# Kernel optimization log

Hardware: AMD Instinct MI355X
Metric: run time of the kernel (lower is better)

The kernel has to match this reference:

```python
import jax, jax.numpy as jnp
import numpy as np

CELL = 4  # 2 ** cell_2_pow, cell_2_pow = 2
EPS = 1e-5


def conv2d(x, w, b):
    # 3x3 conv, padding 1, NCHW / OIHW
    y = jax.lax.conv_general_dilated(
        x, w, window_strides=(1, 1), padding=((1, 1), (1, 1)),
        dimension_numbers=('NCHW', 'OIHW', 'NCHW'))
    return y + b[None, :, None, None]


def setup_inputs() -> dict:
    key = jax.random.key(0)
    ks = jax.random.split(key, 4)
    B, Cc, H, W = 8, 128, 512, 512
    nh, nw = H // CELL, W // CELL  # ctrl spatial must be padded_img / cell_sz
    return dict(
        image_pipe=jax.random.normal(ks[0], (B, 6, H, W), jnp.float32),
        ctrl_pipe=jax.random.normal(ks[1], (B, Cc, nh, nw), jnp.float32),
        w1=jax.random.normal(ks[2], (50, Cc, 3, 3), jnp.float32) * 0.03,
        b1=jnp.zeros((50,), jnp.float32),
        gamma=jnp.ones((50,), jnp.float32),
        beta=jnp.zeros((50,), jnp.float32),
        mean=jnp.zeros((50,), jnp.float32),
        var=jnp.ones((50,), jnp.float32),
        w2=jax.random.normal(ks[3], (18, 50, 3, 3), jnp.float32) * 0.05,
        b2=jnp.zeros((18,), jnp.float32),
    )


def reference(image_pipe, ctrl_pipe, w1, b1, gamma, beta, mean, var, w2, b2):
    cs = CELL
    B, C6, H, W = image_pipe.shape
    # conv_condense: Conv(Cc->50) -> ReLU -> BatchNorm2d(50, inference) -> Conv(50->18)
    h = jax.nn.relu(conv2d(ctrl_pipe, w1, b1))
    scale = gamma * jax.lax.rsqrt(var + EPS)
    h = (h - mean[None, :, None, None]) * scale[None, :, None, None] + beta[None, :, None, None]
    cond = conv2d(h, w2, b2)  # [B, 18, nh, nw]
    nh, nw = cond.shape[-2], cond.shape[-1]

    padH = (-H) % cs
    padW = (-W) % cs
    rH, rW = H + padH, W + padW
    # F.pad(img, (cell, padW+cell, cell, padH+cell)): left/right then top/bottom
    img = jnp.pad(image_pipe, ((0, 0), (0, 0), (cs, padH + cs), (cs, padW + cs)))

    # 9 cell-strided shifted views; torch loop order: i over width (outer), j over height (inner)
    stack = jnp.stack(
        [img[:, :, j * cs:j * cs + rH, i * cs:i * cs + rW]
         for i in range(3) for j in range(3)], axis=-1)  # [B, 6, rH, rW, 9]
    stack = stack.reshape(B, 2, 3, rH, rW, 9)  # 2 groups of 3 channels

    # per-pixel dynamic 9-tap weights, constant within each cs x cs cell
    wts = cond.reshape(B, 2, 9, nh, nw)
    wts = jnp.repeat(jnp.repeat(wts, cs, axis=3), cs, axis=4)  # [B, 2, 9, rH, rW]

    out = jnp.einsum('bgchwk,bgkhw->bgchw', stack, wts)  # weighted neighborhood sum
    out = out.reshape(B, 6, rH, rW)[:, :, :H, :W]
    return out
```

## Files before the change

kernel.cpp:

```cpp
#include <hip/hip_runtime.h>

typedef __attribute__((ext_vector_type(8))) short short8;
typedef __attribute__((ext_vector_type(4))) float floatx4;

__device__ __forceinline__ unsigned short f2bf(float f) {
    union { float f; unsigned int u; } v; v.f = f;
    unsigned int r = (v.u + 0x7fffu + ((v.u >> 16) & 1u)) >> 16;
    return (unsigned short)r;
}

__device__ __forceinline__ void gload_lds16(const void* g, void* l) {
    __builtin_amdgcn_global_load_lds(
        (const __attribute__((address_space(1))) unsigned int*)g,
        (__attribute__((address_space(3))) unsigned int*)l, 16, 0, 0);
}

__global__ __launch_bounds__(256) void transpose_kernel(
    const float* __restrict__ ctrl, unsigned short* __restrict__ ctrlT)
{
    __shared__ unsigned short tile[64 * 66];
    const int t = threadIdx.x;
    const int x0 = blockIdx.x * 64, ci0 = blockIdx.y * 64;
    const int b = blockIdx.z >> 7, y = blockIdx.z & 127;
#pragma unroll
    for (int it = 0; it < 4; it++) {
        int ci_l = it * 16 + (t >> 4);
        int x_l = (t & 15) * 4;
        const float4 v = *(const float4*)&ctrl[(((size_t)b * 128 + ci0 + ci_l) * 128 + y) * 128 + x0 + x_l];
        tile[(x_l + 0) * 66 + ci_l] = f2bf(v.x);
        tile[(x_l + 1) * 66 + ci_l] = f2bf(v.y);
        tile[(x_l + 2) * 66 + ci_l] = f2bf(v.z);
        tile[(x_l + 3) * 66 + ci_l] = f2bf(v.w);
    }
    __syncthreads();
#pragma unroll
    for (int it = 0; it < 2; it++) {
        int x_l = it * 32 + (t >> 3);
        int ci_l = (t & 7) * 8;
        const unsigned int* p = (const unsigned int*)&tile[x_l * 66 + ci_l];
        uint4 u = make_uint4(p[0], p[1], p[2], p[3]);
        *(uint4*)&ctrlT[(((size_t)b * 130 + (y + 1)) * 130 + (x0 + x_l + 1)) * 128 + ci0 + ci_l] = u;
    }
}

__global__ __launch_bounds__(256) void prep_w_kernel(
    const float* __restrict__ w1, const float* __restrict__ w2,
    unsigned short* __restrict__ w1p, unsigned short* __restrict__ w2p,
    unsigned short* __restrict__ ctrlT, unsigned short* __restrict__ hbuf)
{
    int i = blockIdx.x * 256 + threadIdx.x;
    if (i < 73728) {
        int ci = i & 31; int t2 = i >> 5; int co = t2 & 63; int t3 = t2 >> 6;
        int tap = t3 % 9; int c4 = t3 / 9;
        float v = 0.f;
        if (co < 50) v = w1[((size_t)co * 128 + c4 * 32 + ci) * 9 + tap];
        w1p[i] = f2bf(v);
    } else if (i < 92160) {
        int j = i - 73728;
        int ci = j & 31; int t2 = j >> 5; int co = t2 & 31; int t3 = t2 >> 5;
        int tap = t3 % 9; int c4 = t3 / 9;
        int cig = c4 * 32 + ci;
        float v = 0.f;
        if (co < 18 && cig < 50) v = w2[((size_t)co * 50 + cig) * 9 + tap];
        w2p[j] = f2bf(v);
    } else if (i < 158208) {
        int k = i - 92160;
        int b = k / 8256, r = k % 8256;
        int px = r >> 4, u4 = r & 15;
        int Y, X;
        if (px < 130)      { Y = 0;        X = px; }
        else if (px < 260) { Y = 129;      X = px - 130; }
        else if (px < 388) { Y = px - 259; X = 0; }
        else               { Y = px - 387; X = 129; }
        *(uint4*)&ctrlT[(((size_t)b * 130 + Y) * 130 + X) * 128 + u4 * 8] = make_uint4(0, 0, 0, 0);
    } else {
        int k = i - 158208;
        int b = k / 4128, r = k % 4128;
        int px = r >> 3, u4 = r & 7;
        int Y, X;
        if (px < 130)      { Y = 0;        X = px; }
        else if (px < 260) { Y = 129;      X = px - 130; }
        else if (px < 388) { Y = px - 259; X = 0; }
        else               { Y = px - 387; X = 129; }
        *(uint4*)&hbuf[(((size_t)b * 130 + Y) * 130 + X) * 64 + u4 * 8] = make_uint4(0, 0, 0, 0);
    }
}

__global__ __launch_bounds__(256) void conv1_mfma(
    const unsigned short* __restrict__ xT, const unsigned short* __restrict__ w1p,
    const float* __restrict__ b1, const float* __restrict__ gamma,
    const float* __restrict__ beta, const float* __restrict__ mean,
    const float* __restrict__ var, unsigned short* __restrict__ h)
{
    __shared__ unsigned short in_s[1344 * 8];
    __shared__ unsigned short w_s[2304 * 8];
    const int tid = threadIdx.x;
    const int x0 = blockIdx.x * 16, y0 = blockIdx.y * 16, b = blockIdx.z;
    const int wid = tid >> 6, lane = tid & 63;
    const int ln = lane & 15, q = lane >> 4;

    floatx4 acc[4][4];
#pragma unroll
    for (int mt = 0; mt < 4; mt++)
#pragma unroll
        for (int nt = 0; nt < 4; nt++) acc[mt][nt] = (floatx4)(0.f);

    for (int c4 = 0; c4 < 4; c4++) {
#pragma unroll
        for (int it = 0; it < 6; it++) {
            const int cbase = it * 256 + wid * 64;
            if (cbase < 1296) {
                int j = cbase + lane; if (j > 1295) j = 1295;
                const int p = j >> 2, s = j & 3;
                const int Y = y0 + p / 18, X = x0 + p % 18;
                gload_lds16(&xT[(((size_t)b * 130 + Y) * 130 + X) * 128 + c4 * 32 + s * 8],
                            &in_s[(size_t)cbase * 8]);
            }
        }
        const unsigned short* wsrc = &w1p[(size_t)c4 * 2304 * 8];
#pragma unroll
        for (int it = 0; it < 9; it++) {
            const int cbase = it * 256 + wid * 64;
            gload_lds16(&wsrc[(size_t)(cbase + lane) * 8], &w_s[(size_t)cbase * 8]);
        }
        __syncthreads();

#pragma unroll
        for (int tap = 0; tap < 9; tap++) {
            const int dy = tap / 3, dx = tap % 3;
            short8 a[4];
#pragma unroll
            for (int mt = 0; mt < 4; mt++)
                a[mt] = *(const short8*)&in_s[(((wid * 4 + mt + dy) * 18 + ln + dx) * 4 + q) * 8];
#pragma unroll
            for (int nt = 0; nt < 4; nt++) {
                short8 bf = *(const short8*)&w_s[((tap * 64 + nt * 16 + ln) * 4 + q) * 8];
#pragma unroll
                for (int mt = 0; mt < 4; mt++)
                    acc[mt][nt] = __builtin_amdgcn_mfma_f32_16x16x32_bf16(a[mt], bf, acc[mt][nt], 0, 0, 0);
            }
        }
        __syncthreads();
    }

#pragma unroll
    for (int nt = 0; nt < 4; nt++) {
        int co = nt * 16 + ln;
        bool real = co < 50;
        float sc = 0.f, mn = 0.f, bt = 0.f, bs = 0.f;
        if (real) {
            sc = gamma[co] * rsqrtf(var[co] + 1e-5f);
            mn = mean[co]; bt = beta[co]; bs = b1[co];
        }
#pragma unroll
        for (int mt = 0; mt < 4; mt++) {
            int gy = y0 + wid * 4 + mt;
#pragma unroll
            for (int r = 0; r < 4; r++) {
                int px = q * 4 + r;
                float v = 0.f;
                if (real) {
                    float tv = fmaxf(acc[mt][nt][r] + bs, 0.f);
                    v = (tv - mn) * sc + bt;
                }
                h[(((size_t)b * 130 + (gy + 1)) * 130 + (x0 + px + 1)) * 64 + co] = f2bf(v);
            }
        }
    }
}

__global__ __launch_bounds__(256) void conv2_mfma(
    const unsigned short* __restrict__ hT, const unsigned short* __restrict__ w2p,
    const float* __restrict__ b2, float* __restrict__ cond)
{
    __shared__ unsigned short in_s[1344 * 8];
    __shared__ unsigned short w_s[1152 * 8];
    const int tid = threadIdx.x;
    const int x0 = blockIdx.x * 16, y0 = blockIdx.y * 16, b = blockIdx.z;
    const int wid = tid >> 6, lane = tid & 63;
    const int ln = lane & 15, q = lane >> 4;

    floatx4 acc[4][2];
#pragma unroll
    for (int mt = 0; mt < 4; mt++)
#pragma unroll
        for (int nt = 0; nt < 2; nt++) acc[mt][nt] = (floatx4)(0.f);

    for (int c4 = 0; c4 < 2; c4++) {
#pragma unroll
        for (int it = 0; it < 6; it++) {
            const int cbase = it * 256 + wid * 64;
            if (cbase < 1296) {
                int j = cbase + lane; if (j > 1295) j = 1295;
                const int p = j >> 2, s = j & 3;
                const int Y = y0 + p / 18, X = x0 + p % 18;
                gload_lds16(&hT[(((size_t)b * 130 + Y) * 130 + X) * 64 + c4 * 32 + s * 8],
                            &in_s[(size_t)cbase * 8]);
            }
        }
        const unsigned short* wsrc = &w2p[(size_t)c4 * 1152 * 8];
#pragma unroll
        for (int it = 0; it < 5; it++) {
            const int cbase = it * 256 + wid * 64;
            if (cbase < 1152)
                gload_lds16(&wsrc[(size_t)(cbase + lane) * 8], &w_s[(size_t)cbase * 8]);
        }
        __syncthreads();

#pragma unroll
        for (int tap = 0; tap < 9; tap++) {
            const int dy = tap / 3, dx = tap % 3;
            short8 a[4];
#pragma unroll
            for (int mt = 0; mt < 4; mt++)
                a[mt] = *(const short8*)&in_s[(((wid * 4 + mt + dy) * 18 + ln + dx) * 4 + q) * 8];
#pragma unroll
            for (int nt = 0; nt < 2; nt++) {
                short8 bf = *(const short8*)&w_s[((tap * 32 + nt * 16 + ln) * 4 + q) * 8];
#pragma unroll
                for (int mt = 0; mt < 4; mt++)
                    acc[mt][nt] = __builtin_amdgcn_mfma_f32_16x16x32_bf16(a[mt], bf, acc[mt][nt], 0, 0, 0);
            }
        }
        __syncthreads();
    }

#pragma unroll
    for (int nt = 0; nt < 2; nt++) {
        int co = nt * 16 + ln;
        if (co < 18) {
            float bs = b2[co];
            int gch = co / 9, k = co % 9;
            int iw = k / 3, jy = k % 3;
#pragma unroll
            for (int mt = 0; mt < 4; mt++) {
                int gy = y0 + wid * 4 + mt;
#pragma unroll
                for (int r = 0; r < 4; r++) {
                    int px = q * 4 + r;
                    cond[((((size_t)b * 2 + gch) * 128 + gy) * 128 + (x0 + px)) * 12 + jy * 4 + iw]
                        = acc[mt][nt][r] + bs;
                }
            }
        }
    }
}

__global__ __launch_bounds__(256) void apply_kernel(
    const float* __restrict__ img, const float* __restrict__ cond,
    float* __restrict__ out)
{
    const int hwid = blockIdx.x;
    const int lid = (hwid & 7) * 512 + (hwid >> 3);
    const int bx = lid & 1, by = (lid >> 1) & 127, bz = lid >> 8;

    const int tid = threadIdx.x;
    const int xl = tid & 63, s = tid >> 6;
    const int x4 = bx * 64 + xl;
    const int o = by * 4 + s;
    const int b = bz >> 1, g = bz & 1;
    const int xo = x4 * 4;

    const float* cw = &cond[((((size_t)b * 2 + g) * 128 + by) * 128 + x4) * 12];
    float4 w0 = *(const float4*)&cw[0];
    float4 w1 = *(const float4*)&cw[4];
    float4 w2 = *(const float4*)&cw[8];

    float4 C[3][3], L[3][3], R[3][3];
    const bool lok = (x4 > 0), rok_x = (x4 < 127);
#pragma unroll
    for (int jy = 0; jy < 3; jy++) {
        const int r = o - 4 + 4 * jy;
        const bool rk = (r >= 0) && (r < 512);
#pragma unroll
        for (int cc = 0; cc < 3; cc++) {
            C[jy][cc] = make_float4(0.f, 0.f, 0.f, 0.f);
            L[jy][cc] = make_float4(0.f, 0.f, 0.f, 0.f);
            R[jy][cc] = make_float4(0.f, 0.f, 0.f, 0.f);
            if (rk) {
                const float* rp = &img[((((size_t)b * 6 + g * 3 + cc) * 512) + r) * 512];
                C[jy][cc] = *(const float4*)&rp[xo];
                if (lok)   L[jy][cc] = *(const float4*)&rp[xo - 4];
                if (rok_x) R[jy][cc] = *(const float4*)&rp[xo + 4];
            }
        }
    }

    float4 acc[3];
#pragma unroll
    for (int cc = 0; cc < 3; cc++) acc[cc] = make_float4(0.f, 0.f, 0.f, 0.f);

#pragma unroll
    for (int jy = 0; jy < 3; jy++) {
        const float4 wj = (jy == 0) ? w0 : (jy == 1) ? w1 : w2;
#pragma unroll
        for (int cc = 0; cc < 3; cc++) {
            const float4 l = L[jy][cc], c = C[jy][cc], r = R[jy][cc];
            acc[cc].x += l.x * wj.x + c.x * wj.y + r.x * wj.z;
            acc[cc].y += l.y * wj.x + c.y * wj.y + r.y * wj.z;
            acc[cc].z += l.z * wj.x + c.z * wj.y + r.z * wj.z;
            acc[cc].w += l.w * wj.x + c.w * wj.y + r.w * wj.z;
        }
    }

#pragma unroll
    for (int cc = 0; cc < 3; cc++)
        *(float4*)&out[((((size_t)b * 6 + g * 3 + cc) * 512) + o) * 512 + xo] = acc[cc];
}

extern "C" void kernel_launch(void* const* d_in, const int* in_sizes, int n_in,
                              void* d_out, int out_size, void* d_ws, size_t ws_size,
                              hipStream_t stream)
{
    const float* img   = (const float*)d_in[0];
    const float* ctrl  = (const float*)d_in[1];
    const float* w1    = (const float*)d_in[2];
    const float* b1    = (const float*)d_in[3];
    const float* gamma = (const float*)d_in[4];
    const float* beta  = (const float*)d_in[5];
    const float* mean  = (const float*)d_in[6];
    const float* var   = (const float*)d_in[7];
    const float* w2    = (const float*)d_in[8];
    const float* b2    = (const float*)d_in[9];
    float* out = (float*)d_out;

    char* ws = (char*)d_ws;
    unsigned short* ctrlT = (unsigned short*)ws;
    unsigned short* hbuf  = (unsigned short*)(ws + 34611200);
    float*          cond  = (float*)(ws + 51916800);
    unsigned short* w1p   = (unsigned short*)(ws + 64499712);
    unsigned short* w2p   = (unsigned short*)(ws + 64647168);

    transpose_kernel<<<dim3(2, 2, 1024), 256, 0, stream>>>(ctrl, ctrlT);
    prep_w_kernel<<<747, 256, 0, stream>>>(w1, w2, w1p, w2p, ctrlT, hbuf);
    conv1_mfma<<<dim3(8, 8, 8), 256, 0, stream>>>(ctrlT, w1p, b1, gamma, beta, mean, var, hbuf);
    conv2_mfma<<<dim3(8, 8, 8), 256, 0, stream>>>(hbuf, w2p, b2, cond);
    apply_kernel<<<4096, 256, 0, stream>>>(img, cond, out);
}
```

Measured before the change: 225.9 us.

## Fuse ctrl transpose and bf16 conversion into conv1 input staging

Drops the separate transpose kernel and its padded bf16 NHWC buffer. conv1 now reads the fp32 NCHW ctrl tensor directly, does the halo zero padding and bf16 conversion in registers, and writes a channel-interleaved tile into LDS. This removes one launch and a full write-plus-read round trip of the intermediate. In exchange the staging uses plain global loads and scalar LDS stores instead of async global-to-LDS loads, and each block rereads overlapping halo columns. It also adds a launch-bounds occupancy hint.

```diff
diff --git a/kernel.cpp b/kernel.cpp
--- a/kernel.cpp
+++ b/kernel.cpp
@@ -15,38 +15,10 @@
         (__attribute__((address_space(3))) unsigned int*)l, 16, 0, 0);
 }
 
-__global__ __launch_bounds__(256) void transpose_kernel(
-    const float* __restrict__ ctrl, unsigned short* __restrict__ ctrlT)
-{
-    __shared__ unsigned short tile[64 * 66];
-    const int t = threadIdx.x;
-    const int x0 = blockIdx.x * 64, ci0 = blockIdx.y * 64;
-    const int b = blockIdx.z >> 7, y = blockIdx.z & 127;
-#pragma unroll
-    for (int it = 0; it < 4; it++) {
-        int ci_l = it * 16 + (t >> 4);
-        int x_l = (t & 15) * 4;
-        const float4 v = *(const float4*)&ctrl[(((size_t)b * 128 + ci0 + ci_l) * 128 + y) * 128 + x0 + x_l];
-        tile[(x_l + 0) * 66 + ci_l] = f2bf(v.x);
-        tile[(x_l + 1) * 66 + ci_l] = f2bf(v.y);
-        tile[(x_l + 2) * 66 + ci_l] = f2bf(v.z);
-        tile[(x_l + 3) * 66 + ci_l] = f2bf(v.w);
-    }
-    __syncthreads();
-#pragma unroll
-    for (int it = 0; it < 2; it++) {
-        int x_l = it * 32 + (t >> 3);
-        int ci_l = (t & 7) * 8;
-        const unsigned int* p = (const unsigned int*)&tile[x_l * 66 + ci_l];
-        uint4 u = make_uint4(p[0], p[1], p[2], p[3]);
-        *(uint4*)&ctrlT[(((size_t)b * 130 + (y + 1)) * 130 + (x0 + x_l + 1)) * 128 + ci0 + ci_l] = u;
-    }
-}
-
 __global__ __launch_bounds__(256) void prep_w_kernel(
     const float* __restrict__ w1, const float* __restrict__ w2,
     unsigned short* __restrict__ w1p, unsigned short* __restrict__ w2p,
-    unsigned short* __restrict__ ctrlT, unsigned short* __restrict__ hbuf)
+    unsigned short* __restrict__ hbuf)
 {
     int i = blockIdx.x * 256 + threadIdx.x;
     if (i < 73728) {
@@ -63,18 +35,8 @@
         float v = 0.f;
         if (co < 18 && cig < 50) v = w2[((size_t)co * 50 + cig) * 9 + tap];
         w2p[j] = f2bf(v);
-    } else if (i < 158208) {
+    } else {
         int k = i - 92160;
-        int b = k / 8256, r = k % 8256;
-        int px = r >> 4, u4 = r & 15;
-        int Y, X;
-        if (px < 130)      { Y = 0;        X = px; }
-        else if (px < 260) { Y = 129;      X = px - 130; }
-        else if (px < 388) { Y = px - 259; X = 0; }
-        else               { Y = px - 387; X = 129; }
-        *(uint4*)&ctrlT[(((size_t)b * 130 + Y) * 130 + X) * 128 + u4 * 8] = make_uint4(0, 0, 0, 0);
-    } else {
-        int k = i - 158208;
         int b = k / 4128, r = k % 4128;
         int px = r >> 3, u4 = r & 7;
         int Y, X;
@@ -86,13 +48,13 @@
     }
 }
 
-__global__ __launch_bounds__(256) void conv1_mfma(
-    const unsigned short* __restrict__ xT, const unsigned short* __restrict__ w1p,
+__global__ __launch_bounds__(256, 2) void conv1_mfma(
+    const float* __restrict__ ctrl, const unsigned short* __restrict__ w1p,
     const float* __restrict__ b1, const float* __restrict__ gamma,
     const float* __restrict__ beta, const float* __restrict__ mean,
     const float* __restrict__ var, unsigned short* __restrict__ h)
 {
-    __shared__ unsigned short in_s[1344 * 8];
+    __shared__ unsigned short in_s[324 * 32];
     __shared__ unsigned short w_s[2304 * 8];
     const int tid = threadIdx.x;
     const int x0 = blockIdx.x * 16, y0 = blockIdx.y * 16, b = blockIdx.z;
@@ -106,23 +68,39 @@
         for (int nt = 0; nt < 4; nt++) acc[mt][nt] = (floatx4)(0.f);
 
     for (int c4 = 0; c4 < 4; c4++) {
-#pragma unroll
-        for (int it = 0; it < 6; it++) {
-            const int cbase = it * 256 + wid * 64;
-            if (cbase < 1296) {
-                int j = cbase + lane; if (j > 1295) j = 1295;
-                const int p = j >> 2, s = j & 3;
-                const int Y = y0 + p / 18, X = x0 + p % 18;
-                gload_lds16(&xT[(((size_t)b * 130 + Y) * 130 + X) * 128 + c4 * 32 + s * 8],
-                            &in_s[(size_t)cbase * 8]);
-            }
-        }
         const unsigned short* wsrc = &w1p[(size_t)c4 * 2304 * 8];
 #pragma unroll
         for (int it = 0; it < 9; it++) {
             const int cbase = it * 256 + wid * 64;
             gload_lds16(&wsrc[(size_t)(cbase + lane) * 8], &w_s[(size_t)cbase * 8]);
         }
+#pragma unroll
+        for (int r = 0; r < 3; r++) {
+            const int i = r * 256 + tid;
+            const bool ok = i < 576;
+            const int row = i >> 5, ci = i & 31;
+            const int gy = y0 - 1 + row;
+            float4 wv[6];
+#pragma unroll
+            for (int f = 0; f < 6; f++) {
+                const int xs = x0 - 4 + f * 4;
+                wv[f] = make_float4(0.f, 0.f, 0.f, 0.f);
+                if (ok && gy >= 0 && gy < 128 && xs >= 0 && xs < 125)
+                    wv[f] = *(const float4*)&ctrl[(((size_t)b * 128 + c4 * 32 + ci) * 128 + gy) * 128 + xs];
+            }
+            if (ok) {
+                float va[24];
+#pragma unroll
+                for (int f = 0; f < 6; f++) {
+                    va[4 * f + 0] = wv[f].x; va[4 * f + 1] = wv[f].y;
+                    va[4 * f + 2] = wv[f].z; va[4 * f + 3] = wv[f].w;
+                }
+                unsigned short* dst = &in_s[(row * 18) * 32 + ci];
+#pragma unroll
+                for (int k = 0; k < 18; k++)
+                    dst[k * 32] = f2bf(va[k + 3]);
+            }
+        }
         __syncthreads();
 
 #pragma unroll
@@ -131,7 +109,7 @@
             short8 a[4];
 #pragma unroll
             for (int mt = 0; mt < 4; mt++)
-                a[mt] = *(const short8*)&in_s[(((wid * 4 + mt + dy) * 18 + ln + dx) * 4 + q) * 8];
+                a[mt] = *(const short8*)&in_s[((wid * 4 + mt + dy) * 18 + ln + dx) * 32 + q * 8];
 #pragma unroll
             for (int nt = 0; nt < 4; nt++) {
                 short8 bf = *(const short8*)&w_s[((tap * 64 + nt * 16 + ln) * 4 + q) * 8];
@@ -325,15 +303,13 @@
     float* out = (float*)d_out;
 
     char* ws = (char*)d_ws;
-    unsigned short* ctrlT = (unsigned short*)ws;
-    unsigned short* hbuf  = (unsigned short*)(ws + 34611200);
-    float*          cond  = (float*)(ws + 51916800);
-    unsigned short* w1p   = (unsigned short*)(ws + 64499712);
-    unsigned short* w2p   = (unsigned short*)(ws + 64647168);
-
-    transpose_kernel<<<dim3(2, 2, 1024), 256, 0, stream>>>(ctrl, ctrlT);
-    prep_w_kernel<<<747, 256, 0, stream>>>(w1, w2, w1p, w2p, ctrlT, hbuf);
-    conv1_mfma<<<dim3(8, 8, 8), 256, 0, stream>>>(ctrlT, w1p, b1, gamma, beta, mean, var, hbuf);
+    unsigned short* hbuf  = (unsigned short*)ws;
+    float*          cond  = (float*)(ws + 17305600);
+    unsigned short* w1p   = (unsigned short*)(ws + 29888512);
+    unsigned short* w2p   = (unsigned short*)(ws + 30035968);
+
+    prep_w_kernel<<<489, 256, 0, stream>>>(w1, w2, w1p, w2p, hbuf);
+    conv1_mfma<<<dim3(8, 8, 8), 256, 0, stream>>>(ctrl, w1p, b1, gamma, beta, mean, var, hbuf);
     conv2_mfma<<<dim3(8, 8, 8), 256, 0, stream>>>(hbuf, w2p, b2, cond);
     apply_kernel<<<4096, 256, 0, stream>>>(img, cond, out);
 }
```

Result: no change. 224.7 us (-0.5%).
